# Performance work log

Measured on AMD Instinct MI355X. Metric: run time of the kernel, lower is better.

## Reference

```python
import jax, jax.numpy as jnp
import numpy as np

N = 100000      # nodes
DEG = 16        # fixed out-degree -> nnz = N*DEG (static for jit)
NNZ = N * DEG
IN_DIM, HID, OUT = 256, 64, 64


def setup_inputs() -> dict:
    key = jax.random.key(0)
    k1, k2, k3, k4, k5 = jax.random.split(key, 5)
    X = jax.random.normal(k1, (N, IN_DIM), dtype=jnp.float32)
    W1 = jax.random.normal(k2, (IN_DIM, HID), dtype=jnp.float32) / np.sqrt(IN_DIM)
    W2 = jax.random.normal(k3, (HID, OUT), dtype=jnp.float32) / np.sqrt(HID)
    vals = jax.random.uniform(k4, (NNZ,), dtype=jnp.float32)
    rowptr = (jnp.arange(N + 1, dtype=jnp.int32) * DEG)  # fixed-degree CSR
    colind = jax.random.randint(k5, (NNZ,), 0, N, dtype=jnp.int32)
    return {"X": X, "W1": W1, "W2": W2, "vals": vals,
            "rowptr": rowptr, "colind": colind}


def spmm_csr(rowptr, colind, vals, B):
    """CSR SpMM: out[i] = sum_{j in row i} vals[j] * B[colind[j]]."""
    deg = rowptr[1:] - rowptr[:-1]                      # [N]
    rows = jnp.repeat(jnp.arange(N, dtype=jnp.int32), deg,
                      total_repeat_length=NNZ)           # [NNZ]
    gathered = vals[:, None] * B[colind]                 # [NNZ, F]
    return jax.ops.segment_sum(gathered, rows, num_segments=N)


def reference(X, W1, W2, vals, rowptr, colind):
    h = X @ W1                        # lin1 (no bias)
    h = spmm_csr(rowptr, colind, vals, h)   # A @ h
    h = jax.nn.relu(h)
    out = h @ W2                      # lin2 (no bias)
    out = spmm_csr(rowptr, colind, vals, out)  # A @ out
    return out
```

## Files before the change

### kernel.cpp

```cpp
#include <hip/hip_runtime.h>
#include <hip/hip_bf16.h>

#define N_NODES 100000
#define DEG 16
#define NT16 6250
#define NG64 1563
#define G1_BLOCKS 782
#define G1_WSTRIDE (G1_BLOCKS * 4)

typedef __attribute__((ext_vector_type(8))) short short8;
typedef __attribute__((ext_vector_type(4))) float f32x4;
typedef __attribute__((ext_vector_type(4))) float f4raw;
typedef __attribute__((ext_vector_type(4))) int   i4raw;
typedef __attribute__((ext_vector_type(4))) unsigned u4raw;

__device__ inline unsigned short f2bf(float f) {
    union { float f; unsigned u; } v; v.f = f;
    unsigned u = v.u;
    u += 0x7FFFu + ((u >> 16) & 1u);
    return (unsigned short)(u >> 16);
}
__device__ inline unsigned pk2bf(float a, float b) {
    union { __hip_bfloat162 b2; unsigned u; } v;
    v.b2 = __float22bfloat162_rn(make_float2(a, b));
    return v.u;
}
__device__ inline float bflo(unsigned u) {
    union { unsigned u; float f; } v; v.u = u << 16; return v.f;
}
__device__ inline float bfhi(unsigned u) {
    union { unsigned u; float f; } v; v.u = u & 0xFFFF0000u; return v.f;
}

__global__ __launch_bounds__(256) void gemm1_k256(const float* __restrict__ X,
                                                  const float* __restrict__ W1,
                                                  unsigned short* __restrict__ h)
{
    __shared__ unsigned short wfrag[256 * 64];
    __shared__ unsigned short estage[4][16 * 72];

    const int tid  = threadIdx.x;
    const int lane = tid & 63;
    const int wid  = tid >> 6;
    const int q    = lane >> 4;
    const int l16  = lane & 15;

    {
        const int kg = tid >> 2;
        const int cq = tid & 3;
        float4 wr[16];
        #pragma unroll
        for (int r = 0; r < 4; ++r)
            #pragma unroll
            for (int i = 0; i < 4; ++i)
                wr[r * 4 + i] = *(const float4*)(W1 + (kg * 4 + r) * 64 + cq * 16 + i * 4);
        const int kb  = kg >> 3;
        const int lnr = (((kg * 4) >> 3) & 3) * 16;
        const int jb  = (kg * 4) & 7;
        #pragma unroll
        for (int c = 0; c < 16; ++c) {
            ushort4 w4;
            #pragma unroll
            for (int r = 0; r < 4; ++r) {
                float4 v = wr[r * 4 + (c >> 2)];
                float  f = ((c & 3) == 0) ? v.x : ((c & 3) == 1) ? v.y :
                           ((c & 3) == 2) ? v.z : v.w;
                ((unsigned short*)&w4)[r] = f2bf(f);
            }
            *(ushort4*)&wfrag[(((kb * 4) + cq) * 64 + lnr + c) * 8 + jb] = w4;
        }
    }
    __syncthreads();

    const int bpidx = (((l16 << 2) | q) << 2);
    const size_t xoff = (size_t)(lane >> 2) * 256 + (lane & 3) * 8;

    int t = blockIdx.x * 4 + wid;

    f4raw pa[8];
    {
        const float* xb = X + (size_t)t * 16 * 256 + xoff;
        #pragma unroll
        for (int kb = 0; kb < 4; ++kb) {
            pa[2 * kb]     = __builtin_nontemporal_load((const f4raw*)(xb + kb * 32));
            pa[2 * kb + 1] = __builtin_nontemporal_load((const f4raw*)(xb + kb * 32 + 4));
        }
    }

    while (t < NT16) {
        const float* xb = X + (size_t)t * 16 * 256 + xoff;
        f4raw pb[8];
        #pragma unroll
        for (int kb = 4; kb < 8; ++kb) {
            pb[2 * (kb - 4)]     = __builtin_nontemporal_load((const f4raw*)(xb + kb * 32));
            pb[2 * (kb - 4) + 1] = __builtin_nontemporal_load((const f4raw*)(xb + kb * 32 + 4));
        }

        f32x4 a0 = {0,0,0,0}, a1 = {0,0,0,0}, a2 = {0,0,0,0}, a3 = {0,0,0,0};

        #pragma unroll
        for (int kb = 0; kb < 4; ++kb) {
            union { int u[4]; short8 s; } uu;
            uu.u[0] = __builtin_amdgcn_ds_bpermute(bpidx, (int)pk2bf(pa[2*kb].x,   pa[2*kb].y));
            uu.u[1] = __builtin_amdgcn_ds_bpermute(bpidx, (int)pk2bf(pa[2*kb].z,   pa[2*kb].w));
            uu.u[2] = __builtin_amdgcn_ds_bpermute(bpidx, (int)pk2bf(pa[2*kb+1].x, pa[2*kb+1].y));
            uu.u[3] = __builtin_amdgcn_ds_bpermute(bpidx, (int)pk2bf(pa[2*kb+1].z, pa[2*kb+1].w));
            const short8* wp = (const short8*)&wfrag[(size_t)((kb * 4) * 64 + lane) * 8];
            a0 = __builtin_amdgcn_mfma_f32_16x16x32_bf16(uu.s, wp[0 * 64], a0, 0, 0, 0);
            a1 = __builtin_amdgcn_mfma_f32_16x16x32_bf16(uu.s, wp[1 * 64], a1, 0, 0, 0);
            a2 = __builtin_amdgcn_mfma_f32_16x16x32_bf16(uu.s, wp[2 * 64], a2, 0, 0, 0);
            a3 = __builtin_amdgcn_mfma_f32_16x16x32_bf16(uu.s, wp[3 * 64], a3, 0, 0, 0);
        }

        const int tn = t + G1_WSTRIDE;
        if (tn < NT16) {
            const float* xn = X + (size_t)tn * 16 * 256 + xoff;
            #pragma unroll
            for (int kb = 0; kb < 4; ++kb) {
                pa[2 * kb]     = __builtin_nontemporal_load((const f4raw*)(xn + kb * 32));
                pa[2 * kb + 1] = __builtin_nontemporal_load((const f4raw*)(xn + kb * 32 + 4));
            }
        }

        #pragma unroll
        for (int kb = 4; kb < 8; ++kb) {
            const int i = kb - 4;
            union { int u[4]; short8 s; } uu;
            uu.u[0] = __builtin_amdgcn_ds_bpermute(bpidx, (int)pk2bf(pb[2*i].x,   pb[2*i].y));
            uu.u[1] = __builtin_amdgcn_ds_bpermute(bpidx, (int)pk2bf(pb[2*i].z,   pb[2*i].w));
            uu.u[2] = __builtin_amdgcn_ds_bpermute(bpidx, (int)pk2bf(pb[2*i+1].x, pb[2*i+1].y));
            uu.u[3] = __builtin_amdgcn_ds_bpermute(bpidx, (int)pk2bf(pb[2*i+1].z, pb[2*i+1].w));
            const short8* wp = (const short8*)&wfrag[(size_t)((kb * 4) * 64 + lane) * 8];
            a0 = __builtin_amdgcn_mfma_f32_16x16x32_bf16(uu.s, wp[0 * 64], a0, 0, 0, 0);
            a1 = __builtin_amdgcn_mfma_f32_16x16x32_bf16(uu.s, wp[1 * 64], a1, 0, 0, 0);
            a2 = __builtin_amdgcn_mfma_f32_16x16x32_bf16(uu.s, wp[2 * 64], a2, 0, 0, 0);
            a3 = __builtin_amdgcn_mfma_f32_16x16x32_bf16(uu.s, wp[3 * 64], a3, 0, 0, 0);
        }

        unsigned short* st = estage[wid];
        #pragma unroll
        for (int r = 0; r < 4; ++r) {
            int rr = (q * 4 + r) * 72 + l16;
            st[rr + 0 * 16] = f2bf(a0[r]);
            st[rr + 1 * 16] = f2bf(a1[r]);
            st[rr + 2 * 16] = f2bf(a2[r]);
            st[rr + 3 * 16] = f2bf(a3[r]);
        }
        #pragma unroll
        for (int i = 0; i < 4; ++i) {
            int row = i * 4 + q;
            uint2 v = *(const uint2*)&st[row * 72 + l16 * 4];
            *(uint2*)(h + (size_t)(t * 16 + row) * 64 + l16 * 4) = v;
        }
        t = tn;
    }
}

__device__ inline void gather_row8(const unsigned short* __restrict__ B,
                                   const int* __restrict__ ci,
                                   const float* __restrict__ vv,
                                   int j8, float* __restrict__ acc)
{
    #pragma unroll
    for (int b = 0; b < 2; ++b) {
        i4raw c0 = __builtin_nontemporal_load((const i4raw*)ci + 2 * b);
        i4raw c1 = __builtin_nontemporal_load((const i4raw*)ci + 2 * b + 1);
        f4raw v0 = __builtin_nontemporal_load((const f4raw*)vv + 2 * b);
        f4raw v1 = __builtin_nontemporal_load((const f4raw*)vv + 2 * b + 1);
        uint4 g0 = *(const uint4*)(B + (size_t)c0.x * 64 + j8 * 8);
        uint4 g1 = *(const uint4*)(B + (size_t)c0.y * 64 + j8 * 8);
        uint4 g2 = *(const uint4*)(B + (size_t)c0.z * 64 + j8 * 8);
        uint4 g3 = *(const uint4*)(B + (size_t)c0.w * 64 + j8 * 8);
        uint4 g4 = *(const uint4*)(B + (size_t)c1.x * 64 + j8 * 8);
        uint4 g5 = *(const uint4*)(B + (size_t)c1.y * 64 + j8 * 8);
        uint4 g6 = *(const uint4*)(B + (size_t)c1.z * 64 + j8 * 8);
        uint4 g7 = *(const uint4*)(B + (size_t)c1.w * 64 + j8 * 8);
#define ACC8(g, s) \
        acc[0] += (s) * bflo((g).x); acc[1] += (s) * bfhi((g).x); \
        acc[2] += (s) * bflo((g).y); acc[3] += (s) * bfhi((g).y); \
        acc[4] += (s) * bflo((g).z); acc[5] += (s) * bfhi((g).z); \
        acc[6] += (s) * bflo((g).w); acc[7] += (s) * bfhi((g).w);
        ACC8(g0, v0.x) ACC8(g1, v0.y) ACC8(g2, v0.z) ACC8(g3, v0.w)
        ACC8(g4, v1.x) ACC8(g5, v1.y) ACC8(g6, v1.z) ACC8(g7, v1.w)
#undef ACC8
    }
}

__global__ __launch_bounds__(256) void spmm_gemm2(const int* __restrict__ colind,
                                                  const float* __restrict__ vals,
                                                  const unsigned short* __restrict__ h,
                                                  const float* __restrict__ W2,
                                                  unsigned short* __restrict__ o1)
{
    __shared__ unsigned short wfrag2[64 * 64];
    __shared__ unsigned short stage[4][16 * 72];

    const int tid  = threadIdx.x;
    const int lane = tid & 63;
    const int wid  = tid >> 6;
    const int q    = lane >> 4;
    const int l16  = lane & 15;

    {
        const int r4 = tid >> 2;
        const int qt = tid & 3;
        float4 wr[4];
        #pragma unroll
        for (int i = 0; i < 4; ++i)
            wr[i] = *(const float4*)(W2 + r4 * 64 + qt * 16 + i * 4);
        const int kb  = r4 >> 5;
        const int j   = r4 & 7;
        const int lnr = ((r4 >> 3) & 3) * 16;
        #pragma unroll
        for (int c = 0; c < 16; ++c) {
            float f = ((c & 3) == 0) ? wr[c >> 2].x :
                      ((c & 3) == 1) ? wr[c >> 2].y :
                      ((c & 3) == 2) ? wr[c >> 2].z : wr[c >> 2].w;
            wfrag2[(((kb * 4) + qt) * 64 + lnr + c) * 8 + j] = f2bf(f);
        }
    }
    __syncthreads();

    const int base = blockIdx.x * 64 + wid * 16;
    unsigned short* st = stage[wid];
    const int rl = lane >> 3;
    const int j8 = lane & 7;

    #pragma unroll
    for (int p = 0; p < 2; ++p) {
        int lr  = p * 8 + rl;
        int row = base + lr;
        int rc  = row < N_NODES ? row : N_NODES - 1;
        float acc[8] = {0.f,0.f,0.f,0.f,0.f,0.f,0.f,0.f};
        gather_row8(h, colind + (size_t)rc * DEG, vals + (size_t)rc * DEG, j8, acc);
        uint4 pk;
        pk.x = pk2bf(fmaxf(acc[0], 0.f), fmaxf(acc[1], 0.f));
        pk.y = pk2bf(fmaxf(acc[2], 0.f), fmaxf(acc[3], 0.f));
        pk.z = pk2bf(fmaxf(acc[4], 0.f), fmaxf(acc[5], 0.f));
        pk.w = pk2bf(fmaxf(acc[6], 0.f), fmaxf(acc[7], 0.f));
        *(uint4*)&st[lr * 72 + j8 * 8] = pk;
    }

    f32x4 a0 = {0,0,0,0}, a1 = {0,0,0,0}, a2 = {0,0,0,0}, a3 = {0,0,0,0};
    #pragma unroll
    for (int kb = 0; kb < 2; ++kb) {
        short8 af = *(const short8*)&st[l16 * 72 + kb * 32 + q * 8];
        const short8* wp = (const short8*)&wfrag2[(size_t)((kb * 4) * 64 + lane) * 8];
        a0 = __builtin_amdgcn_mfma_f32_16x16x32_bf16(af, wp[0 * 64], a0, 0, 0, 0);
        a1 = __builtin_amdgcn_mfma_f32_16x16x32_bf16(af, wp[1 * 64], a1, 0, 0, 0);
        a2 = __builtin_amdgcn_mfma_f32_16x16x32_bf16(af, wp[2 * 64], a2, 0, 0, 0);
        a3 = __builtin_amdgcn_mfma_f32_16x16x32_bf16(af, wp[3 * 64], a3, 0, 0, 0);
    }
    #pragma unroll
    for (int r = 0; r < 4; ++r) {
        int rr = (q * 4 + r) * 72 + l16;
        st[rr + 0 * 16] = f2bf(a0[r]);
        st[rr + 1 * 16] = f2bf(a1[r]);
        st[rr + 2 * 16] = f2bf(a2[r]);
        st[rr + 3 * 16] = f2bf(a3[r]);
    }
    #pragma unroll
    for (int i = 0; i < 4; ++i) {
        int row = base + i * 4 + q;
        if (row < N_NODES) {
            uint2 v = *(const uint2*)&st[(i * 4 + q) * 72 + l16 * 4];
            *(uint2*)(o1 + (size_t)row * 64 + l16 * 4) = v;
        }
    }
}

__global__ __launch_bounds__(256) void spmm_out(const int* __restrict__ colind,
                                                const float* __restrict__ vals,
                                                const unsigned short* __restrict__ B,
                                                float* __restrict__ out)
{
    const int tid  = threadIdx.x;
    const int lane = tid & 63;
    const int wid  = tid >> 6;
    const int rl   = lane >> 3;
    const int j8   = lane & 7;
    const int row  = blockIdx.x * 32 + wid * 8 + rl;

    float acc[8] = {0.f,0.f,0.f,0.f,0.f,0.f,0.f,0.f};
    gather_row8(B, colind + (size_t)row * DEG, vals + (size_t)row * DEG, j8, acc);

    f4raw lo = { acc[0], acc[1], acc[2], acc[3] };
    f4raw hi = { acc[4], acc[5], acc[6], acc[7] };
    float* op = out + (size_t)row * 64 + j8 * 8;
    *(f4raw*)op       = lo;
    *(f4raw*)(op + 4) = hi;
}

extern "C" void kernel_launch(void* const* d_in, const int* in_sizes, int n_in,
                              void* d_out, int out_size, void* d_ws, size_t ws_size,
                              hipStream_t stream) {
    const float* X      = (const float*)d_in[0];
    const float* W1     = (const float*)d_in[1];
    const float* W2     = (const float*)d_in[2];
    const float* vals   = (const float*)d_in[3];
    const int*   colind = (const int*)d_in[5];
    float*       out    = (float*)d_out;

    unsigned short* h  = (unsigned short*)d_ws;
    unsigned short* o1 = h + (size_t)N_NODES * 64;

    hipLaunchKernelGGL(gemm1_k256, dim3(G1_BLOCKS), dim3(256), 0, stream, X, W1, h);
    hipLaunchKernelGGL(spmm_gemm2, dim3(NG64), dim3(256), 0, stream,
                       colind, vals, h, W2, o1);
    hipLaunchKernelGGL(spmm_out, dim3(N_NODES / 32), dim3(256), 0, stream,
                       colind, vals, o1, out);
}
```

Before: 232.2 us.

## Fuse SpMM-GEMM2 and output SpMM into one persistent kernel with grid barrier

```diff
diff --git a/kernel.cpp b/kernel.cpp
--- a/kernel.cpp
+++ b/kernel.cpp
@@ -5,8 +5,10 @@
 #define DEG 16
 #define NT16 6250
 #define NG64 1563
+#define NB32 3125
 #define G1_BLOCKS 782
 #define G1_WSTRIDE (G1_BLOCKS * 4)
+#define FGRID 1024
 
 typedef __attribute__((ext_vector_type(8))) short short8;
 typedef __attribute__((ext_vector_type(4))) float f32x4;
@@ -34,7 +36,8 @@
 
 __global__ __launch_bounds__(256) void gemm1_k256(const float* __restrict__ X,
                                                   const float* __restrict__ W1,
-                                                  unsigned short* __restrict__ h)
+                                                  unsigned short* __restrict__ h,
+                                                  unsigned* __restrict__ barrier_ctr)
 {
     __shared__ unsigned short wfrag[256 * 64];
     __shared__ unsigned short estage[4][16 * 72];
@@ -44,6 +47,8 @@
     const int wid  = tid >> 6;
     const int q    = lane >> 4;
     const int l16  = lane & 15;
+
+    if (blockIdx.x == 0 && tid == 0) *barrier_ctr = 0;
 
     {
         const int kg = tid >> 2;
@@ -186,11 +191,13 @@
     }
 }
 
-__global__ __launch_bounds__(256) void spmm_gemm2(const int* __restrict__ colind,
-                                                  const float* __restrict__ vals,
-                                                  const unsigned short* __restrict__ h,
-                                                  const float* __restrict__ W2,
-                                                  unsigned short* __restrict__ o1)
+__global__ __launch_bounds__(256, 4) void spmm_fused(const int* __restrict__ colind,
+                                                     const float* __restrict__ vals,
+                                                     const unsigned short* __restrict__ h,
+                                                     const float* __restrict__ W2,
+                                                     unsigned short* __restrict__ o1,
+                                                     float* __restrict__ out,
+                                                     unsigned* __restrict__ barrier_ctr)
 {
     __shared__ unsigned short wfrag2[64 * 64];
     __shared__ unsigned short stage[4][16 * 72];
@@ -200,6 +207,8 @@
     const int wid  = tid >> 6;
     const int q    = lane >> 4;
     const int l16  = lane & 15;
+    const int rl   = lane >> 3;
+    const int j8   = lane & 7;
 
     {
         const int r4 = tid >> 2;
@@ -221,74 +230,75 @@
     }
     __syncthreads();
 
-    const int base = blockIdx.x * 64 + wid * 16;
     unsigned short* st = stage[wid];
-    const int rl = lane >> 3;
-    const int j8 = lane & 7;
-
-    #pragma unroll
-    for (int p = 0; p < 2; ++p) {
-        int lr  = p * 8 + rl;
-        int row = base + lr;
-        int rc  = row < N_NODES ? row : N_NODES - 1;
+
+    for (int vb = blockIdx.x; vb < NG64; vb += FGRID) {
+        const int base = vb * 64 + wid * 16;
+
+        #pragma unroll
+        for (int p = 0; p < 2; ++p) {
+            int lr  = p * 8 + rl;
+            int row = base + lr;
+            int rc  = row < N_NODES ? row : N_NODES - 1;
+            float acc[8] = {0.f,0.f,0.f,0.f,0.f,0.f,0.f,0.f};
+            gather_row8(h, colind + (size_t)rc * DEG, vals + (size_t)rc * DEG, j8, acc);
+            uint4 pk;
+            pk.x = pk2bf(fmaxf(acc[0], 0.f), fmaxf(acc[1], 0.f));
+            pk.y = pk2bf(fmaxf(acc[2], 0.f), fmaxf(acc[3], 0.f));
+            pk.z = pk2bf(fmaxf(acc[4], 0.f), fmaxf(acc[5], 0.f));
+            pk.w = pk2bf(fmaxf(acc[6], 0.f), fmaxf(acc[7], 0.f));
+            *(uint4*)&st[lr * 72 + j8 * 8] = pk;
+        }
+
+        f32x4 a0 = {0,0,0,0}, a1 = {0,0,0,0}, a2 = {0,0,0,0}, a3 = {0,0,0,0};
+        #pragma unroll
+        for (int kb = 0; kb < 2; ++kb) {
+            short8 af = *(const short8*)&st[l16 * 72 + kb * 32 + q * 8];
+            const short8* wp = (const short8*)&wfrag2[(size_t)((kb * 4) * 64 + lane) * 8];
+            a0 = __builtin_amdgcn_mfma_f32_16x16x32_bf16(af, wp[0 * 64], a0, 0, 0, 0);
+            a1 = __builtin_amdgcn_mfma_f32_16x16x32_bf16(af, wp[1 * 64], a1, 0, 0, 0);
+            a2 = __builtin_amdgcn_mfma_f32_16x16x32_bf16(af, wp[2 * 64], a2, 0, 0, 0);
+            a3 = __builtin_amdgcn_mfma_f32_16x16x32_bf16(af, wp[3 * 64], a3, 0, 0, 0);
+        }
+        #pragma unroll
+        for (int r = 0; r < 4; ++r) {
+            int rr = (q * 4 + r) * 72 + l16;
+            st[rr + 0 * 16] = f2bf(a0[r]);
+            st[rr + 1 * 16] = f2bf(a1[r]);
+            st[rr + 2 * 16] = f2bf(a2[r]);
+            st[rr + 3 * 16] = f2bf(a3[r]);
+        }
+        #pragma unroll
+        for (int i = 0; i < 4; ++i) {
+            int row = base + i * 4 + q;
+            if (row < N_NODES) {
+                uint2 v = *(const uint2*)&st[(i * 4 + q) * 72 + l16 * 4];
+                *(uint2*)(o1 + (size_t)row * 64 + l16 * 4) = v;
+            }
+        }
+    }
+
+    __syncthreads();
+    if (tid == 0) {
+        __hip_atomic_fetch_add(barrier_ctr, 1u, __ATOMIC_ACQ_REL, __HIP_MEMORY_SCOPE_AGENT);
+        while (__hip_atomic_load(barrier_ctr, __ATOMIC_ACQUIRE, __HIP_MEMORY_SCOPE_AGENT) < FGRID) {
+            __builtin_amdgcn_s_sleep(32);
+        }
+    }
+    __syncthreads();
+    __threadfence();
+
+    for (int vb = blockIdx.x; vb < NB32; vb += FGRID) {
+        const int row = vb * 32 + wid * 8 + rl;
         float acc[8] = {0.f,0.f,0.f,0.f,0.f,0.f,0.f,0.f};
-        gather_row8(h, colind + (size_t)rc * DEG, vals + (size_t)rc * DEG, j8, acc);
-        uint4 pk;
-        pk.x = pk2bf(fmaxf(acc[0], 0.f), fmaxf(acc[1], 0.f));
-        pk.y = pk2bf(fmaxf(acc[2], 0.f), fmaxf(acc[3], 0.f));
-        pk.z = pk2bf(fmaxf(acc[4], 0.f), fmaxf(acc[5], 0.f));
-        pk.w = pk2bf(fmaxf(acc[6], 0.f), fmaxf(acc[7], 0.f));
-        *(uint4*)&st[lr * 72 + j8 * 8] = pk;
-    }
-
-    f32x4 a0 = {0,0,0,0}, a1 = {0,0,0,0}, a2 = {0,0,0,0}, a3 = {0,0,0,0};
-    #pragma unroll
-    for (int kb = 0; kb < 2; ++kb) {
-        short8 af = *(const short8*)&st[l16 * 72 + kb * 32 + q * 8];
-        const short8* wp = (const short8*)&wfrag2[(size_t)((kb * 4) * 64 + lane) * 8];
-        a0 = __builtin_amdgcn_mfma_f32_16x16x32_bf16(af, wp[0 * 64], a0, 0, 0, 0);
-        a1 = __builtin_amdgcn_mfma_f32_16x16x32_bf16(af, wp[1 * 64], a1, 0, 0, 0);
-        a2 = __builtin_amdgcn_mfma_f32_16x16x32_bf16(af, wp[2 * 64], a2, 0, 0, 0);
-        a3 = __builtin_amdgcn_mfma_f32_16x16x32_bf16(af, wp[3 * 64], a3, 0, 0, 0);
-    }
-    #pragma unroll
-    for (int r = 0; r < 4; ++r) {
-        int rr = (q * 4 + r) * 72 + l16;
-        st[rr + 0 * 16] = f2bf(a0[r]);
-        st[rr + 1 * 16] = f2bf(a1[r]);
-        st[rr + 2 * 16] = f2bf(a2[r]);
-        st[rr + 3 * 16] = f2bf(a3[r]);
-    }
-    #pragma unroll
-    for (int i = 0; i < 4; ++i) {
-        int row = base + i * 4 + q;
-        if (row < N_NODES) {
-            uint2 v = *(const uint2*)&st[(i * 4 + q) * 72 + l16 * 4];
-            *(uint2*)(o1 + (size_t)row * 64 + l16 * 4) = v;
-        }
-    }
-}
-
-__global__ __launch_bounds__(256) void spmm_out(const int* __restrict__ colind,
-                                                const float* __restrict__ vals,
-                                                const unsigned short* __restrict__ B,
-                                                float* __restrict__ out)
-{
-    const int tid  = threadIdx.x;
-    const int lane = tid & 63;
-    const int wid  = tid >> 6;
-    const int rl   = lane >> 3;
-    const int j8   = lane & 7;
-    const int row  = blockIdx.x * 32 + wid * 8 + rl;
-
-    float acc[8] = {0.f,0.f,0.f,0.f,0.f,0.f,0.f,0.f};
-    gather_row8(B, colind + (size_t)row * DEG, vals + (size_t)row * DEG, j8, acc);
-
-    f4raw lo = { acc[0], acc[1], acc[2], acc[3] };
-    f4raw hi = { acc[4], acc[5], acc[6], acc[7] };
-    float* op = out + (size_t)row * 64 + j8 * 8;
-    *(f4raw*)op       = lo;
-    *(f4raw*)(op + 4) = hi;
+        gather_row8(o1, colind + (size_t)row * DEG, vals + (size_t)row * DEG, j8, acc);
+
+        f4raw lo = { acc[0], acc[1], acc[2], acc[3] };
+        f4raw hi = { acc[4], acc[5], acc[6], acc[7] };
+        float* op = out + (size_t)row * 64 + j8 * 8;
+        *(f4raw*)op       = lo;
+        *(f4raw*)(op + 4) = hi;
+    }
 }
 
 extern "C" void kernel_launch(void* const* d_in, const int* in_sizes, int n_in,
@@ -303,10 +313,9 @@
 
     unsigned short* h  = (unsigned short*)d_ws;
     unsigned short* o1 = h + (size_t)N_NODES * 64;
-
-    hipLaunchKernelGGL(gemm1_k256, dim3(G1_BLOCKS), dim3(256), 0, stream, X, W1, h);
-    hipLaunchKernelGGL(spmm_gemm2, dim3(NG64), dim3(256), 0, stream,
-                       colind, vals, h, W2, o1);
-    hipLaunchKernelGGL(spmm_out, dim3(N_NODES / 32), dim3(256), 0, stream,
-                       colind, vals, o1, out);
-}
+    unsigned* barrier_ctr = (unsigned*)(o1 + (size_t)N_NODES * 64);
+
+    hipLaunchKernelGGL(gemm1_k256, dim3(G1_BLOCKS), dim3(256), 0, stream, X, W1, h, barrier_ctr);
+    hipLaunchKernelGGL(spmm_fused, dim3(FGRID), dim3(256), 0, stream,
+                       colind, vals, h, W2, o1, out, barrier_ctr);
+}
```

Result: slower. 440.4 us (+89.7%).
